# Optimization experiments

Measured on AMD Instinct MI355X. Metric: run time of the kernel, lower is better.

Reference implementation:

```python
import jax, jax.numpy as jnp
import numpy as np

N_NODES = 50000
N_EDGES = 800000
NUM_FEATURES = 128
HIDDEN = 128
NUM_CLASSES = 32


def gcn_conv(x, src, dst, n, W, b):
    loop = jnp.arange(n)
    s = jnp.concatenate([src, loop])
    d = jnp.concatenate([dst, loop])
    deg = jax.ops.segment_sum(jnp.ones_like(d, dtype=x.dtype), d, num_segments=n)
    dinv = jnp.where(deg > 0, jax.lax.rsqrt(deg), 0.0)
    norm = dinv[s] * dinv[d]                      # [E+n]
    h = x @ W                                     # [n, out]
    msg = h[s] * norm[:, None]                    # gather + scale
    out = jax.ops.segment_sum(msg, d, num_segments=n)  # scatter-add
    return out + b


def setup_inputs() -> dict:
    key = jax.random.key(0)
    ks = jax.random.split(key, 9)
    x = jax.random.normal(ks[0], (N_NODES, NUM_FEATURES), dtype=jnp.float32)
    edge_index = jax.random.randint(ks[1], (2, N_EDGES), 0, N_NODES, dtype=jnp.int64)
    sc1 = 1.0 / np.sqrt(NUM_FEATURES)
    sc2 = 1.0 / np.sqrt(HIDDEN)
    W1 = jax.random.uniform(ks[2], (NUM_FEATURES, HIDDEN), jnp.float32, -sc1, sc1)
    b1 = jnp.zeros((HIDDEN,), jnp.float32)
    W2 = jax.random.uniform(ks[3], (HIDDEN, HIDDEN), jnp.float32, -sc2, sc2)
    b2 = jnp.zeros((HIDDEN,), jnp.float32)
    Wfc = jax.random.uniform(ks[4], (HIDDEN, NUM_CLASSES), jnp.float32, -sc2, sc2)
    bfc = jax.random.uniform(ks[5], (NUM_CLASSES,), jnp.float32, -sc2, sc2)
    return {"x": x, "edge_index": edge_index, "W1": W1, "b1": b1,
            "W2": W2, "b2": b2, "Wfc": Wfc, "bfc": bfc}


def reference(x, edge_index, W1, b1, W2, b2, Wfc, bfc):
    n = x.shape[0]
    src, dst = edge_index[0], edge_index[1]
    h = jax.nn.relu(gcn_conv(x, src, dst, n, W1, b1))
    h = jax.nn.relu(gcn_conv(h, src, dst, n, W2, b2))
    # global_mean_pool with batch = zeros -> mean over all nodes, shape [1, HIDDEN]
    pooled = jnp.mean(h, axis=0, keepdims=True)
    return pooled @ Wfc + bfc  # [1, NUM_CLASSES]
```

## Files before the change

kernel.cpp:

```cpp
#include <hip/hip_runtime.h>
#include <stdint.h>

#define FEAT 128
#define ECH 2048
#define CAP 200000
#define SCB 512

typedef short bf16x8 __attribute__((ext_vector_type(8)));
typedef float f32x4 __attribute__((ext_vector_type(4)));
typedef float f32x2 __attribute__((ext_vector_type(2)));

__device__ __forceinline__ float bfs(unsigned short u) {
    uint32_t t = ((uint32_t)u) << 16;
    return __builtin_bit_cast(float, t);
}
__device__ __forceinline__ unsigned short f2bf(float f) {
    uint32_t u = __builtin_bit_cast(uint32_t, f);
    u += 0x7fffu + ((u >> 16) & 1u);
    return (unsigned short)(u >> 16);
}

__device__ __forceinline__ void acc8(int2 u, float m, float* a) {
    f32x2 t;
    t = __builtin_amdgcn_cvt_pk_f32_fp8(u.x, false);
    a[0] = fmaf(m, t.x, a[0]); a[1] = fmaf(m, t.y, a[1]);
    t = __builtin_amdgcn_cvt_pk_f32_fp8(u.x, true);
    a[2] = fmaf(m, t.x, a[2]); a[3] = fmaf(m, t.y, a[3]);
    t = __builtin_amdgcn_cvt_pk_f32_fp8(u.y, false);
    a[4] = fmaf(m, t.x, a[4]); a[5] = fmaf(m, t.y, a[5]);
    t = __builtin_amdgcn_cvt_pk_f32_fp8(u.y, true);
    a[6] = fmaf(m, t.x, a[6]); a[7] = fmaf(m, t.y, a[7]);
}

__launch_bounds__(256)
__global__ void k_prep(const int* __restrict__ ei,
                       int* __restrict__ dstb, int* __restrict__ srcb,
                       int* __restrict__ bcnt, int* __restrict__ deg,
                       int E, int n, int psz, int NE,
                       const void* W1, const void* W2,
                       const void* b1, const void* b2,
                       const void* Wfc, const void* bfc,
                       unsigned short* Wth1, unsigned short* Wth2,
                       float* b1f, float* b2f, float* Wfcf, float* bfcf) {
    int t = threadIdx.x;

    if ((int)blockIdx.x >= NE) {
        __shared__ int hits;
        int blk = blockIdx.x - NE;
        const void* sampsrc = (blk < 32) ? W1 : (blk < 64 ? W2 : Wfc);
        const uint32_t* samp = (const uint32_t*)sampsrc;
        if (t == 0) hits = 0;
        __syncthreads();
        unsigned ew = (samp[t] >> 7) & 0xFFu;
        unsigned long long bl = __ballot(ew >= 0x60u && ew <= 0x90u);
        if ((t & 63) == 0) atomicAdd(&hits, (int)__popcll(bl));
        __syncthreads();
        int isbf = (2 * hits > 256);

        if (blk < 64) {
            const void* W = (blk < 32) ? W1 : W2;
            unsigned short* th = (blk < 32) ? Wth1 : Wth2;
            int base = (blk & 31) * 512;
            #pragma unroll
            for (int j = 0; j < 2; j++) {
                int idx = base + t * 2 + j;
                int nn = idx >> 7, k = idx & 127;
                int si = k * 128 + nn;
                float f = isbf ? bfs(((const unsigned short*)W)[si])
                               : ((const float*)W)[si];
                th[nn * 128 + k] = f2bf(f);
            }
        } else {
            int i = (blk - 64) * 256 + t;
            if (i >= 4384) return;
            const void* src; float* dst; int off;
            if (i < 128)       { src = b1;  dst = b1f;  off = i; }
            else if (i < 256)  { src = b2;  dst = b2f;  off = i - 128; }
            else if (i < 4352) { src = Wfc; dst = Wfcf; off = i - 256; }
            else               { src = bfc; dst = bfcf; off = i - 4352; }
            dst[off] = isbf ? bfs(((const unsigned short*)src)[off])
                            : ((const float*)src)[off];
        }
        return;
    }

    __shared__ int lflag;
    __shared__ int cnt[8], lofs[8], gbase[8];
    __shared__ int stage_s[ECH];
    __shared__ int stage_d[ECH];
    __shared__ char sb[ECH];
    if (t < 128) {
        int di = blockIdx.x * 128 + t;
        if (di < n) deg[di] = 0;
    }
    if (t == 0) lflag = 0;
    if (t < 8) cnt[t] = 0;
    __syncthreads();
    if (ei[1 + 2 * t] != 0) atomicOr(&lflag, 1);
    __syncthreads();
    int is32 = lflag;

    int base = blockIdx.x * ECH;
    int s[8], d[8], p[8], slot[8];
    #pragma unroll
    for (int j = 0; j < 8; j++) {
        int e = base + j * 256 + t;
        int ss = 0, dd = 0;
        if (e < E) {
            ss = is32 ? ei[e]     : ei[2 * e];
            dd = is32 ? ei[E + e] : ei[2 * E + 2 * e];
            if ((unsigned)ss >= (unsigned)n) ss = 0;
            if ((unsigned)dd >= (unsigned)n) dd = 0;
            int pp = dd / psz;
            if (pp > 7) pp = 7;
            p[j] = pp;
            slot[j] = atomicAdd(&cnt[pp], 1);
        } else p[j] = -1;
        s[j] = ss; d[j] = dd;
    }
    __syncthreads();
    if (t == 0) {
        int acc = 0;
        #pragma unroll
        for (int i = 0; i < 8; i++) { lofs[i] = acc; acc += cnt[i]; }
    }
    __syncthreads();
    if (t < 8) gbase[t] = atomicAdd(&bcnt[t], cnt[t]);
    __syncthreads();
    #pragma unroll
    for (int j = 0; j < 8; j++) {
        if (p[j] >= 0) {
            int pos = lofs[p[j]] + slot[j];
            stage_s[pos] = s[j];
            stage_d[pos] = d[j];
            sb[pos] = (char)p[j];
        }
    }
    __syncthreads();
    int tot = lofs[7] + cnt[7];
    for (int i = t; i < tot; i += 256) {
        int pp = sb[i];
        int off = gbase[pp] + (i - lofs[pp]);
        if (off < CAP) {
            dstb[pp * CAP + off] = stage_d[i];
            srcb[pp * CAP + off] = stage_s[i];
        }
    }
}

__launch_bounds__(256)
__global__ void k_degp(const int* __restrict__ dstb, const int* __restrict__ bcnt,
                       int* __restrict__ deg) {
    int p = blockIdx.x & 7;
    int nb = gridDim.x >> 3;
    int cnt = bcnt[p]; if (cnt > CAP) cnt = CAP;
    const int* db = dstb + p * CAP;
    for (int i = (blockIdx.x >> 3) * 256 + threadIdx.x; i < cnt; i += nb * 256)
        atomicAdd(&deg[db[i]], 1);
}

__global__ void k_bsum(const int* __restrict__ deg, int* __restrict__ bsum,
                       float* __restrict__ dinv, int n) {
    __shared__ int ws[4];
    int t = threadIdx.x, lane = t & 63, w = t >> 6;
    int idx = blockIdx.x * 256 + t;
    int v = (idx < n) ? deg[idx] : 0;
    if (idx < n) dinv[idx] = rsqrtf((float)(v + 1));
    int r = v;
    #pragma unroll
    for (int off = 32; off > 0; off >>= 1) r += __shfl_down(r, off, 64);
    if (lane == 0) ws[w] = r;
    __syncthreads();
    if (t == 0) bsum[blockIdx.x] = ws[0] + ws[1] + ws[2] + ws[3];
}

__launch_bounds__(256)
__global__ void k_bapply2(const int* __restrict__ deg, const int* __restrict__ bsum,
                          int* __restrict__ row_ptr, int* __restrict__ cursor,
                          int n, int nb) {
    __shared__ int wred[4];
    __shared__ int wsum[4];
    __shared__ int boffs;
    int b = blockIdx.x, t = threadIdx.x, lane = t & 63, w = t >> 6;

    int pv = (t < b && t < nb) ? bsum[t] : 0;
    #pragma unroll
    for (int off = 32; off > 0; off >>= 1) pv += __shfl_down(pv, off, 64);
    if (lane == 0) wred[w] = pv;
    __syncthreads();
    if (t == 0) boffs = wred[0] + wred[1] + wred[2] + wred[3];
    __syncthreads();

    int idx = b * 256 + t;
    int v = (idx < n) ? deg[idx] : 0;
    int s = v;
    #pragma unroll
    for (int off = 1; off < 64; off <<= 1) {
        int x = __shfl_up(s, off, 64);
        if (lane >= off) s += x;
    }
    if (lane == 63) wsum[w] = s;
    __syncthreads();
    if (t == 0) {
        int acc = 0;
        #pragma unroll
        for (int i = 0; i < 4; i++) { int x = wsum[i]; wsum[i] = acc; acc += x; }
    }
    __syncthreads();
    int ex = boffs + s - v + wsum[w];
    if (idx < n) {
        row_ptr[idx] = ex;
        cursor[idx]  = ex;
    }
    if (idx == n - 1) row_ptr[n] = ex + v;
}

__device__ __forceinline__ void gemm_body(const void* __restrict__ X,
                                          const unsigned short* __restrict__ Wth,
                                          const float* __restrict__ dinv,
                                          uint32_t* __restrict__ hs8,
                                          int n, int tile, int l,
                                          unsigned char* __restrict__ ldsrow) {
    int quad = l >> 4;
    int m16 = l & 15;
    int r0 = tile * 16;

    unsigned ew = (((const uint32_t*)X)[l] >> 7) & 0xFFu;
    unsigned long long bl = __ballot(ew >= 0x60u && ew <= 0x90u);
    int isbf = ((int)__popcll(bl) * 2 > 64) ? 1 : 0;

    int ra = r0 + m16;
    if (ra > n - 1) ra = n - 1;
    bf16x8 ah[4];
    if (isbf) {
        const int4* Xv = (const int4*)X;
        #pragma unroll
        for (int kt = 0; kt < 4; kt++)
            ah[kt] = __builtin_bit_cast(bf16x8, Xv[ra * 16 + kt * 4 + quad]);
    } else {
        const float4* Xf = (const float4*)X;
        #pragma unroll
        for (int kt = 0; kt < 4; kt++) {
            int jj = kt * 4 + quad;
            float4 fa = Xf[ra * 32 + jj * 2];
            float4 fb = Xf[ra * 32 + jj * 2 + 1];
            float v[8] = {fa.x, fa.y, fa.z, fa.w, fb.x, fb.y, fb.z, fb.w};
            bf16x8 h;
            #pragma unroll
            for (int j = 0; j < 8; j++) h[j] = (short)f2bf(v[j]);
            ah[kt] = h;
        }
    }

    float dv[4];
    #pragma unroll
    for (int reg = 0; reg < 4; reg++) {
        int row = r0 + quad * 4 + reg;
        if (row > n - 1) row = n - 1;
        dv[reg] = dinv[row];
    }

    const int4* Wvh = (const int4*)Wth;
    #pragma unroll
    for (int nt = 0; nt < 8; nt++) {
        f32x4 acc = {0.f, 0.f, 0.f, 0.f};
        int brow = (nt * 16 + m16) * 16;
        #pragma unroll
        for (int kt = 0; kt < 4; kt++) {
            bf16x8 bh = __builtin_bit_cast(bf16x8, Wvh[brow + kt * 4 + quad]);
            acc = __builtin_amdgcn_mfma_f32_16x16x32_bf16(ah[kt], bh, acc, 0, 0, 0);
        }
        #pragma unroll
        for (int reg = 0; reg < 4; reg++) {
            float v = acc[reg] * dv[reg];
            int pk = __builtin_amdgcn_cvt_pk_fp8_f32(v, v, 0, false);
            ldsrow[(quad * 4 + reg) * 128 + nt * 16 + m16] = (unsigned char)(pk & 0xFF);
        }
    }
    __syncthreads();
    const uint32_t* l32 = (const uint32_t*)ldsrow;
    #pragma unroll
    for (int i = 0; i < 8; i++) {
        int idx = i * 64 + l;
        int row = idx >> 5;
        int grow = r0 + row;
        if (grow < n) hs8[grow * 32 + (idx & 31)] = l32[idx];
    }
}

__launch_bounds__(256)
__global__ void k_sg(const int* __restrict__ dstb, const int* __restrict__ srcb,
                     const int* __restrict__ bcnt,
                     int* __restrict__ cursor, int* __restrict__ col, int E,
                     const void* __restrict__ X,
                     const unsigned short* __restrict__ Wth,
                     const float* __restrict__ dinv,
                     uint32_t* __restrict__ hs8, int n) {
    __shared__ unsigned char lds8[4][16 * 128];
    int b = blockIdx.x;
    if (b < SCB) {
        int p = b & 7;
        int nb = SCB >> 3;
        int cnt = bcnt[p]; if (cnt > CAP) cnt = CAP;
        const int* db = dstb + p * CAP;
        const int* sb = srcb + p * CAP;
        for (int i = (b >> 3) * 256 + threadIdx.x; i < cnt; i += nb * 256) {
            int pos = atomicAdd(&cursor[db[i]], 1);
            if ((unsigned)pos < (unsigned)E) col[pos] = sb[i];
        }
        return;
    }
    int wave = threadIdx.x >> 6;
    int l = threadIdx.x & 63;
    gemm_body(X, Wth, dinv, hs8, n, (b - SCB) * 4 + wave, l, lds8[wave]);
}

__launch_bounds__(256)
__global__ void k_agg1gemm2(const unsigned short* __restrict__ hsv,
                            const int* __restrict__ row_ptr,
                            const int* __restrict__ col,
                            const float* __restrict__ dinv,
                            const float* __restrict__ bias,
                            const unsigned short* __restrict__ Wth2,
                            uint32_t* __restrict__ hs8out, int n, int E) {
    __shared__ __align__(16) unsigned short actlds[16 * 136];
    __shared__ unsigned char pack[16 * 128];
    int wave = threadIdx.x >> 6;
    int lane = threadIdx.x & 63;
    int q16 = lane & 15;
    int slot = lane >> 4;
    int tile0 = blockIdx.x * 16;
    const int2* hsw2 = (const int2*)hsv;

    int base_node = tile0 + wave * 4;
    int rp[5];
    #pragma unroll
    for (int k = 0; k < 5; k++) {
        int nn = base_node + k;
        if (nn > n) nn = n;
        rp[k] = row_ptr[nn];
    }
    int nd4[4]; int2 selfw4[4];
    #pragma unroll
    for (int k = 0; k < 4; k++) {
        int node = base_node + k;
        nd4[k] = (node < n) ? node : 0;
        selfw4[k] = hsw2[nd4[k] * 16 + q16];
    }

    #pragma unroll
    for (int i = 0; i < 4; i++) {
        int node = base_node + i;
        bool active = (node < n);
        int nd = nd4[i];

        int e = rp[i];
        int end = active ? rp[i + 1] : e;
        if (e < 0) e = 0;
        if (end > E) end = E;
        if (end < e) end = e;

        float a[8];
        #pragma unroll
        for (int j = 0; j < 8; j++) a[j] = 0.f;
        acc8(selfw4[i], (slot == 0) ? 1.0f : 0.0f, a);

        for (; e + 16 <= end; e += 16) {
            int2 uu[4];
            #pragma unroll
            for (int j = 0; j < 4; j++) {
                unsigned s = (unsigned)col[e + 4 * j + slot];
                if (s >= (unsigned)n) s = 0;
                uu[j] = hsw2[s * 16 + q16];
            }
            #pragma unroll
            for (int j = 0; j < 4; j++) acc8(uu[j], 1.0f, a);
        }
        if (e < end) {
            int2 uu[4];
            #pragma unroll
            for (int j = 0; j < 4; j++) {
                int ej = e + 4 * j + slot;
                int ec = (ej < end) ? ej : (end - 1);
                unsigned s = (unsigned)col[ec];
                if (s >= (unsigned)n) s = 0;
                uu[j] = hsw2[s * 16 + q16];
            }
            #pragma unroll
            for (int j = 0; j < 4; j++) {
                float m = ((e + 4 * j + slot) < end) ? 1.0f : 0.0f;
                acc8(uu[j], m, a);
            }
        }
        #pragma unroll
        for (int j = 0; j < 8; j++) {
            a[j] += __shfl_xor(a[j], 16, 64);
            a[j] += __shfl_xor(a[j], 32, 64);
        }

        if (slot == 0) {
            float dv = dinv[nd];
            const float4* b4 = (const float4*)bias;
            float4 b0 = b4[2 * q16];
            float4 b1q = b4[2 * q16 + 1];
            float r0 = fmaxf(dv * a[0] + b0.x, 0.f);
            float r1 = fmaxf(dv * a[1] + b0.y, 0.f);
            float r2 = fmaxf(dv * a[2] + b0.z, 0.f);
            float r3 = fmaxf(dv * a[3] + b0.w, 0.f);
            float r4 = fmaxf(dv * a[4] + b1q.x, 0.f);
            float r5 = fmaxf(dv * a[5] + b1q.y, 0.f);
            float r6 = fmaxf(dv * a[6] + b1q.z, 0.f);
            float r7 = fmaxf(dv * a[7] + b1q.w, 0.f);
            if (!active) { r0=0.f;r1=0.f;r2=0.f;r3=0.f;r4=0.f;r5=0.f;r6=0.f;r7=0.f; }
            int row = wave * 4 + i;
            uint4 w;
            w.x = (uint32_t)f2bf(r0) | ((uint32_t)f2bf(r1) << 16);
            w.y = (uint32_t)f2bf(r2) | ((uint32_t)f2bf(r3) << 16);
            w.z = (uint32_t)f2bf(r4) | ((uint32_t)f2bf(r5) << 16);
            w.w = (uint32_t)f2bf(r6) | ((uint32_t)f2bf(r7) << 16);
            *(uint4*)&actlds[row * 136 + 8 * q16] = w;
        }
    }
    __syncthreads();

    int quad = lane >> 4;
    int m16 = lane & 15;
    bf16x8 ah[4];
    #pragma unroll
    for (int kt = 0; kt < 4; kt++) {
        const unsigned short* p = &actlds[m16 * 136 + kt * 32 + quad * 8];
        ah[kt] = __builtin_bit_cast(bf16x8, *(const int4*)p);
    }
    float dv4[4];
    #pragma unroll
    for (int reg = 0; reg < 4; reg++) {
        int row = tile0 + quad * 4 + reg;
        if (row > n - 1) row = n - 1;
        dv4[reg] = dinv[row];
    }
    const int4* Wvh = (const int4*)Wth2;
    #pragma unroll
    for (int ntl = 0; ntl < 2; ntl++) {
        int nt = wave * 2 + ntl;
        f32x4 acc = {0.f, 0.f, 0.f, 0.f};
        int brow = (nt * 16 + m16) * 16;
        #pragma unroll
        for (int kt = 0; kt < 4; kt++) {
            bf16x8 bh = __builtin_bit_cast(bf16x8, Wvh[brow + kt * 4 + quad]);
            acc = __builtin_amdgcn_mfma_f32_16x16x32_bf16(ah[kt], bh, acc, 0, 0, 0);
        }
        #pragma unroll
        for (int reg = 0; reg < 4; reg++) {
            float v = acc[reg] * dv4[reg];
            int pk = __builtin_amdgcn_cvt_pk_fp8_f32(v, v, 0, false);
            pack[(quad * 4 + reg) * 128 + nt * 16 + m16] = (unsigned char)(pk & 0xFF);
        }
    }
    __syncthreads();
    const uint32_t* l32 = (const uint32_t*)pack;
    #pragma unroll
    for (int i = 0; i < 2; i++) {
        int idx = i * 256 + threadIdx.x;
        int row = idx >> 5;
        int grow = tile0 + row;
        if (grow < n) hs8out[grow * 32 + (idx & 31)] = l32[idx];
    }
}

__launch_bounds__(256)
__global__ void k_agg(const unsigned short* __restrict__ hsv,
                      const int* __restrict__ row_ptr,
                      const int* __restrict__ col, const float* __restrict__ dinv,
                      const float* __restrict__ bias,
                      float* __restrict__ partial, int n, int E) {
    __shared__ __align__(16) float pl[4][128];
    int wave = threadIdx.x >> 6;
    int lane = threadIdx.x & 63;
    int q16 = lane & 15;
    int slot = lane >> 4;
    int node = blockIdx.x * 4 + wave;
    bool active = (node < n);
    int nd = active ? node : 0;
    const int2* hsw2 = (const int2*)hsv;

    int2 selfw = hsw2[nd * 16 + q16];
    int e = row_ptr[nd];
    int end = active ? row_ptr[nd + 1] : e;
    if (e < 0) e = 0;
    if (end > E) end = E;
    if (end < e) end = e;

    float a[8];
    #pragma unroll
    for (int j = 0; j < 8; j++) a[j] = 0.f;
    acc8(selfw, (slot == 0) ? 1.0f : 0.0f, a);

    for (; e + 16 <= end; e += 16) {
        int2 uu[4];
        #pragma unroll
        for (int j = 0; j < 4; j++) {
            unsigned s = (unsigned)col[e + 4 * j + slot];
            if (s >= (unsigned)n) s = 0;
            uu[j] = hsw2[s * 16 + q16];
        }
        #pragma unroll
        for (int j = 0; j < 4; j++) acc8(uu[j], 1.0f, a);
    }
    if (e < end) {
        int2 uu[4];
        #pragma unroll
        for (int j = 0; j < 4; j++) {
            int ej = e + 4 * j + slot;
            int ec = (ej < end) ? ej : (end - 1);
            unsigned s = (unsigned)col[ec];
            if (s >= (unsigned)n) s = 0;
            uu[j] = hsw2[s * 16 + q16];
        }
        #pragma unroll
        for (int j = 0; j < 4; j++) {
            float m = ((e + 4 * j + slot) < end) ? 1.0f : 0.0f;
            acc8(uu[j], m, a);
        }
    }
    #pragma unroll
    for (int j = 0; j < 8; j++) {
        a[j] += __shfl_xor(a[j], 16, 64);
        a[j] += __shfl_xor(a[j], 32, 64);
    }

    if (slot == 0) {
        float dv = dinv[nd];
        const float4* b4 = (const float4*)bias;
        float4 b0 = b4[2 * q16];
        float4 b1q = b4[2 * q16 + 1];
        float4 ra, rb;
        ra.x = fmaxf(dv * a[0] + b0.x, 0.f);
        ra.y = fmaxf(dv * a[1] + b0.y, 0.f);
        ra.z = fmaxf(dv * a[2] + b0.z, 0.f);
        ra.w = fmaxf(dv * a[3] + b0.w, 0.f);
        rb.x = fmaxf(dv * a[4] + b1q.x, 0.f);
        rb.y = fmaxf(dv * a[5] + b1q.y, 0.f);
        rb.z = fmaxf(dv * a[6] + b1q.z, 0.f);
        rb.w = fmaxf(dv * a[7] + b1q.w, 0.f);
        if (!active) {
            ra.x=0.f;ra.y=0.f;ra.z=0.f;ra.w=0.f;
            rb.x=0.f;rb.y=0.f;rb.z=0.f;rb.w=0.f;
        }
        *(float4*)&pl[wave][8 * q16]     = ra;
        *(float4*)&pl[wave][8 * q16 + 4] = rb;
    }
    __syncthreads();
    int t = threadIdx.x;
    if (t < 128) {
        float ps = pl[0][t] + pl[1][t] + pl[2][t] + pl[3][t];
        partial[blockIdx.x * 128 + t] = ps;
    }
}

__launch_bounds__(256)
__global__ void k_redfinal(const float* __restrict__ partial, float* __restrict__ pooled,
                           int* __restrict__ done,
                           const float* __restrict__ Wfcf, const float* __restrict__ bfcf,
                           const void* __restrict__ x, void* __restrict__ out,
                           int n, int nbrows, int gblocks) {
    __shared__ float red[8][128];
    int t = threadIdx.x;
    int chunk = (nbrows + gblocks - 1) / gblocks;
    int r0 = blockIdx.x * chunk;
    int r1 = r0 + chunk;
    if (r1 > nbrows) r1 = nbrows;

    float4 acc = {0.f, 0.f, 0.f, 0.f};
    const float4* p4 = (const float4*)partial;
    for (int i = r0 * 32 + t; i < r1 * 32; i += 256) {
        float4 v = p4[i];
        acc.x += v.x; acc.y += v.y; acc.z += v.z; acc.w += v.w;
    }
    int g = t >> 5;
    int fb = (t & 31) * 4;
    red[g][fb]     = acc.x;
    red[g][fb + 1] = acc.y;
    red[g][fb + 2] = acc.z;
    red[g][fb + 3] = acc.w;
    __syncthreads();
    if (t < 128) {
        float s = red[0][t] + red[1][t] + red[2][t] + red[3][t]
                + red[4][t] + red[5][t] + red[6][t] + red[7][t];
        atomicAdd(&pooled[t], s);
    }
    __threadfence();
    __shared__ int lastf;
    if (t == 0) lastf = (atomicAdd(done, 1) == gblocks - 1) ? 1 : 0;
    __syncthreads();
    if (!lastf) return;

    __shared__ int hits;
    __shared__ float pv[128];
    if (t == 0) hits = 0;
    __syncthreads();
    unsigned ew = (((const uint32_t*)x)[t] >> 7) & 0xFFu;
    unsigned long long bl = __ballot(ew >= 0x60u && ew <= 0x90u);
    if ((t & 63) == 0) atomicAdd(&hits, (int)__popcll(bl));
    if (t < 128)
        pv[t] = __hip_atomic_load(&pooled[t], __ATOMIC_RELAXED,
                                  __HIP_MEMORY_SCOPE_AGENT);
    __syncthreads();
    int isbf = (2 * hits > 256);
    if (t < 32) {
        float s = 0.f;
        for (int c = 0; c < 128; ++c) s += pv[c] * Wfcf[c * 32 + t];
        s = s * (1.0f / (float)n) + bfcf[t];
        if (isbf) ((unsigned short*)out)[t] = f2bf(s);
        else      ((float*)out)[t] = s;
    }
}


extern "C" void kernel_launch(void* const* d_in, const int* in_sizes, int n_in,
                              void* d_out, int out_size, void* d_ws, size_t ws_size,
                              hipStream_t stream) {
    const void* x   = d_in[0];
    const int*  ei  = (const int*)d_in[1];
    const void* W1  = d_in[2];
    const void* b1  = d_in[3];
    const void* W2  = d_in[4];
    const void* b2  = d_in[5];
    const void* Wfc = d_in[6];
    const void* bfc = d_in[7];

    const int n = in_sizes[0] / FEAT;
    const int E = in_sizes[1] / 2;
    const int nagg = (n + 3) / 4;
    const int ntile = (n + 15) / 16;
    const int psz  = (n + 7) / 8;
    const int nscan = (n + 255) / 256;
    const int NE   = (E + ECH - 1) / ECH;
    const int gemm_grid = (ntile + 3) / 4;

    char* ws = (char*)d_ws;
    uint32_t*       hs8     = (uint32_t*)(ws);
    uint32_t*       hs8b    = (uint32_t*)(ws + 12800000);
    float*          partial = (float*)(ws + 25600000);
    int*            col     = (int*)(ws + 38400000);
    int*            dstb    = (int*)(ws + 41600000);
    int*            srcb    = (int*)(ws + 48000000);
    int*            deg     = (int*)(ws + 54400000);
    int*            row_ptr = (int*)(ws + 54600000);
    int*            cursor  = (int*)(ws + 54800016);
    float*          dinv    = (float*)(ws + 55000016);
    unsigned short* Wth1    = (unsigned short*)(ws + 55200016);
    unsigned short* Wth2    = (unsigned short*)(ws + 55232784);
    float*          b1f     = (float*)(ws + 55265552);
    float*          b2f     = (float*)(ws + 55266064);
    float*          Wfcf    = (float*)(ws + 55266576);
    float*          bfcf    = (float*)(ws + 55282960);
    float*          pooled  = (float*)(ws + 55283088);
    int*            bcnt    = (int*)(ws + 55283600);
    int*            done    = (int*)(ws + 55283632);
    int*            bsum    = (int*)(ws + 55283648);

    if (ws_size < 55284448) return;

    hipMemsetAsync(pooled, 0, 1344, stream);

    k_prep<<<NE + 82, 256, 0, stream>>>(ei, dstb, srcb, bcnt, deg, E, n, psz, NE,
                                        W1, W2, b1, b2, Wfc, bfc,
                                        Wth1, Wth2, b1f, b2f, Wfcf, bfcf);
    k_degp<<<512, 256, 0, stream>>>(dstb, bcnt, deg);
    k_bsum<<<nscan, 256, 0, stream>>>(deg, bsum, dinv, n);
    k_bapply2<<<nscan, 256, 0, stream>>>(deg, bsum, row_ptr, cursor, n, nscan);
    k_sg<<<SCB + gemm_grid, 256, 0, stream>>>(dstb, srcb, bcnt, cursor, col, E,
                                              x, Wth1, dinv, hs8, n);
    k_agg1gemm2<<<ntile, 256, 0, stream>>>((const unsigned short*)hs8, row_ptr,
                                           col, dinv, b1f, Wth2, hs8b, n, E);
    k_agg<<<nagg, 256, 0, stream>>>((const unsigned short*)hs8b, row_ptr, col,
                                    dinv, b2f, partial, n, E);
    k_redfinal<<<100, 256, 0, stream>>>(partial, pooled, done, Wfcf, bfcf,
                                        x, d_out, n, nagg, 100);
}
```

Measured before the change: 262.5 us.

## Drop destination-partitioned edge bucketing and fuse degree counting into prep

Removes the 8-way destination-range bucketing of edges (LDS staging, per-block offsets, global bucket counters) and writes src/dst in original edge order instead. Degree atomics move into the prep kernel, which removes the separate k_degp launch, and deg is now zeroed with a memset. The bucketing existed to give the scatter into CSR cursors locality by destination range. Dropping it saves a kernel launch and the staging work, but the atomics on deg and cursor now hit scattered addresses with less L2 locality.

Result: no change. 259.7 us (-1.1%).

```diff
diff --git a/kernel.cpp b/kernel.cpp
--- a/kernel.cpp
+++ b/kernel.cpp
@@ -3,7 +3,6 @@
 
 #define FEAT 128
 #define ECH 2048
-#define CAP 200000
 #define SCB 512
 
 typedef short bf16x8 __attribute__((ext_vector_type(8)));
@@ -35,8 +34,8 @@
 __launch_bounds__(256)
 __global__ void k_prep(const int* __restrict__ ei,
                        int* __restrict__ dstb, int* __restrict__ srcb,
-                       int* __restrict__ bcnt, int* __restrict__ deg,
-                       int E, int n, int psz, int NE,
+                       int* __restrict__ deg,
+                       int E, int n, int NE,
                        const void* W1, const void* W2,
                        const void* b1, const void* b2,
                        const void* Wfc, const void* bfc,
@@ -85,78 +84,26 @@
     }
 
     __shared__ int lflag;
-    __shared__ int cnt[8], lofs[8], gbase[8];
-    __shared__ int stage_s[ECH];
-    __shared__ int stage_d[ECH];
-    __shared__ char sb[ECH];
-    if (t < 128) {
-        int di = blockIdx.x * 128 + t;
-        if (di < n) deg[di] = 0;
-    }
     if (t == 0) lflag = 0;
-    if (t < 8) cnt[t] = 0;
     __syncthreads();
     if (ei[1 + 2 * t] != 0) atomicOr(&lflag, 1);
     __syncthreads();
     int is32 = lflag;
 
     int base = blockIdx.x * ECH;
-    int s[8], d[8], p[8], slot[8];
     #pragma unroll
     for (int j = 0; j < 8; j++) {
         int e = base + j * 256 + t;
-        int ss = 0, dd = 0;
         if (e < E) {
-            ss = is32 ? ei[e]     : ei[2 * e];
-            dd = is32 ? ei[E + e] : ei[2 * E + 2 * e];
+            int ss = is32 ? ei[e]     : ei[2 * e];
+            int dd = is32 ? ei[E + e] : ei[2 * E + 2 * e];
             if ((unsigned)ss >= (unsigned)n) ss = 0;
             if ((unsigned)dd >= (unsigned)n) dd = 0;
-            int pp = dd / psz;
-            if (pp > 7) pp = 7;
-            p[j] = pp;
-            slot[j] = atomicAdd(&cnt[pp], 1);
-        } else p[j] = -1;
-        s[j] = ss; d[j] = dd;
-    }
-    __syncthreads();
-    if (t == 0) {
-        int acc = 0;
-        #pragma unroll
-        for (int i = 0; i < 8; i++) { lofs[i] = acc; acc += cnt[i]; }
-    }
-    __syncthreads();
-    if (t < 8) gbase[t] = atomicAdd(&bcnt[t], cnt[t]);
-    __syncthreads();
-    #pragma unroll
-    for (int j = 0; j < 8; j++) {
-        if (p[j] >= 0) {
-            int pos = lofs[p[j]] + slot[j];
-            stage_s[pos] = s[j];
-            stage_d[pos] = d[j];
-            sb[pos] = (char)p[j];
-        }
-    }
-    __syncthreads();
-    int tot = lofs[7] + cnt[7];
-    for (int i = t; i < tot; i += 256) {
-        int pp = sb[i];
-        int off = gbase[pp] + (i - lofs[pp]);
-        if (off < CAP) {
-            dstb[pp * CAP + off] = stage_d[i];
-            srcb[pp * CAP + off] = stage_s[i];
-        }
-    }
-}
-
-__launch_bounds__(256)
-__global__ void k_degp(const int* __restrict__ dstb, const int* __restrict__ bcnt,
-                       int* __restrict__ deg) {
-    int p = blockIdx.x & 7;
-    int nb = gridDim.x >> 3;
-    int cnt = bcnt[p]; if (cnt > CAP) cnt = CAP;
-    const int* db = dstb + p * CAP;
-    for (int i = (blockIdx.x >> 3) * 256 + threadIdx.x; i < cnt; i += nb * 256)
-        atomicAdd(&deg[db[i]], 1);
+            srcb[e] = ss;
+            dstb[e] = dd;
+            atomicAdd(&deg[dd], 1);
+        }
+    }
 }
 
 __global__ void k_bsum(const int* __restrict__ deg, int* __restrict__ bsum,
@@ -290,7 +237,6 @@
 
 __launch_bounds__(256)
 __global__ void k_sg(const int* __restrict__ dstb, const int* __restrict__ srcb,
-                     const int* __restrict__ bcnt,
                      int* __restrict__ cursor, int* __restrict__ col, int E,
                      const void* __restrict__ X,
                      const unsigned short* __restrict__ Wth,
@@ -299,14 +245,9 @@
     __shared__ unsigned char lds8[4][16 * 128];
     int b = blockIdx.x;
     if (b < SCB) {
-        int p = b & 7;
-        int nb = SCB >> 3;
-        int cnt = bcnt[p]; if (cnt > CAP) cnt = CAP;
-        const int* db = dstb + p * CAP;
-        const int* sb = srcb + p * CAP;
-        for (int i = (b >> 3) * 256 + threadIdx.x; i < cnt; i += nb * 256) {
-            int pos = atomicAdd(&cursor[db[i]], 1);
-            if ((unsigned)pos < (unsigned)E) col[pos] = sb[i];
+        for (int i = b * 256 + threadIdx.x; i < E; i += SCB * 256) {
+            int pos = atomicAdd(&cursor[dstb[i]], 1);
+            if ((unsigned)pos < (unsigned)E) col[pos] = srcb[i];
         }
         return;
     }
@@ -632,7 +573,6 @@
     const int E = in_sizes[1] / 2;
     const int nagg = (n + 3) / 4;
     const int ntile = (n + 15) / 16;
-    const int psz  = (n + 7) / 8;
     const int nscan = (n + 255) / 256;
     const int NE   = (E + ECH - 1) / ECH;
     const int gemm_grid = (ntile + 3) / 4;
@@ -655,21 +595,20 @@
     float*          Wfcf    = (float*)(ws + 55266576);
     float*          bfcf    = (float*)(ws + 55282960);
     float*          pooled  = (float*)(ws + 55283088);
-    int*            bcnt    = (int*)(ws + 55283600);
     int*            done    = (int*)(ws + 55283632);
     int*            bsum    = (int*)(ws + 55283648);
 
     if (ws_size < 55284448) return;
 
     hipMemsetAsync(pooled, 0, 1344, stream);
-
-    k_prep<<<NE + 82, 256, 0, stream>>>(ei, dstb, srcb, bcnt, deg, E, n, psz, NE,
+    hipMemsetAsync(deg, 0, (size_t)n * 4, stream);
+
+    k_prep<<<NE + 82, 256, 0, stream>>>(ei, dstb, srcb, deg, E, n, NE,
                                         W1, W2, b1, b2, Wfc, bfc,
                                         Wth1, Wth2, b1f, b2f, Wfcf, bfcf);
-    k_degp<<<512, 256, 0, stream>>>(dstb, bcnt, deg);
     k_bsum<<<nscan, 256, 0, stream>>>(deg, bsum, dinv, n);
     k_bapply2<<<nscan, 256, 0, stream>>>(deg, bsum, row_ptr, cursor, n, nscan);
-    k_sg<<<SCB + gemm_grid, 256, 0, stream>>>(dstb, srcb, bcnt, cursor, col, E,
+    k_sg<<<SCB + gemm_grid, 256, 0, stream>>>(dstb, srcb, cursor, col, E,
                                               x, Wth1, dinv, hs8, n);
     k_agg1gemm2<<<ntile, 256, 0, stream>>>((const unsigned short*)hs8, row_ptr,
                                            col, dinv, b1f, Wth2, hs8b, n, E);
```
